# Kernel optimization log

Measured on AMD Instinct MI355X. Metric: run time of the kernel, lower is better.

Reference implementation:

```python
import jax, jax.numpy as jnp
import numpy as np

ATTEN_SIZE = 16
HIDDEN = 512


def setup_inputs() -> dict:
    key = jax.random.key(0)
    ks = jax.random.split(key, 6)
    B, S, D_in, H, D_out = 64, 100, 256, HIDDEN, 256
    # xavier-normal-ish scale for weights
    def xav(k, shape):
        fan_in, fan_out = shape
        std = np.sqrt(2.0 / (fan_in + fan_out))
        return jax.random.normal(k, shape, dtype=jnp.float32) * std
    return {
        "x": jax.random.normal(ks[0], (B, S, D_in), dtype=jnp.float32),
        "W0": xav(ks[1], (D_in, H)),
        "b0": jnp.zeros((1, 1, H), dtype=jnp.float32),
        "Wq": xav(ks[2], (H, H)),
        "Wk": xav(ks[3], (H, H)),
        "Wv": xav(ks[4], (H, H)),
        "W1": xav(ks[5], (H, D_out)),
        "b1": jnp.zeros((1, 1, D_out), dtype=jnp.float32),
    }


def reference(x, W0, b0, Wq, Wk, Wv, W1, b1):
    w = ATTEN_SIZE
    win = 2 * w + 1
    B, S = x.shape[0], x.shape[1]
    # pre-attention MLP layer (atten_layer_index = 1)
    h = jax.nn.relu(x @ W0 + b0)  # [B, S, H]
    # sliding-window neighbor gather, matching pad + roll(k) + stack + slice:
    # x_nei[:, i, k_idx] = padded[:, i + 2w - k_idx]  (reversed window order)
    padded = jnp.pad(h, ((0, 0), (w, w), (0, 0)))  # [B, S+2w, H]
    idx = jnp.arange(S)[:, None] + (2 * w - jnp.arange(win))[None, :]
    x_nei = padded[:, idx]
    q = x_nei @ Wq
    k = x_nei @ Wk
    v = x_nei @ Wv
    d = jnp.einsum('bswh,buh_->bswu'.replace('h_', 'sh'[1] + 'h'), q, k) if False else jnp.einsum('bswh,bsuh->bswu', q, k)
    d = d / jnp.sqrt(jnp.float32(HIDDEN))
    alpha = jax.nn.softmax(d, axis=-1)
    wv = jnp.einsum('bswu,bsuh->bswh', alpha, v)
    out = wv.sum(axis=2)  # sum over window rows -> [B, S, H]
    y = jax.nn.relu(out @ W1 + b1)  # [B, S, D_out]
    return y, alpha.reshape(B * S, win, win)
```

## Files before the change

kernel.cpp:

```cpp
#include <hip/hip_runtime.h>

typedef __bf16 bf16x8 __attribute__((ext_vector_type(8)));
typedef float f32x4 __attribute__((ext_vector_type(4)));
typedef unsigned int u32;

__device__ __forceinline__ unsigned short f2bf(float f) {
  unsigned int u = __float_as_uint(f);
  u += 0x7FFFu + ((u >> 16) & 1u);
  return (unsigned short)(u >> 16);
}
__device__ __forceinline__ float bf2f(unsigned short s) {
  return __uint_as_float(((unsigned int)s) << 16);
}

__device__ __forceinline__ void gload16(const void* g, void* l) {
  __builtin_amdgcn_global_load_lds(
      (const __attribute__((address_space(1))) u32*)g,
      (__attribute__((address_space(3))) u32*)l, 16, 0, 0);
}

__global__ __launch_bounds__(256) void prep_kernel(
    const float* __restrict__ x, const float* __restrict__ W0,
    const float* __restrict__ Wq, const float* __restrict__ Wk,
    const float* __restrict__ Wv, const float* __restrict__ W1,
    unsigned short* __restrict__ xb, unsigned short* __restrict__ w0t,
    unsigned short* __restrict__ wqkvt, unsigned short* __restrict__ w1t)
{
  __shared__ float tile[32][33];
  const int bid = blockIdx.x, tid = threadIdx.x;
  if (bid < 1600) {
    long i = (long)bid * 1024 + tid * 4;
    float4 v = *(const float4*)(x + i);
    ushort4 o = {f2bf(v.x), f2bf(v.y), f2bf(v.z), f2bf(v.w)};
    *(ushort4*)(xb + i) = o;
    return;
  }
  int id = bid - 1600;
  const float* src; unsigned short* dst;
  int N, DLD, k0, n0, drow0;
  if (id < 128) {
    src = W0; N = 512; dst = w0t; DLD = 256;
    k0 = (id >> 4) * 32; n0 = (id & 15) * 32; drow0 = n0;
  } else if (id < 896) {
    int id1 = id - 128, which = id1 >> 8, rem = id1 & 255;
    src = (which == 0) ? Wq : (which == 1) ? Wk : Wv;
    N = 512; dst = wqkvt; DLD = 512;
    k0 = (rem >> 4) * 32; n0 = (rem & 15) * 32; drow0 = which * 512 + n0;
  } else {
    int id2 = id - 896;
    src = W1; N = 256; dst = w1t; DLD = 512;
    k0 = (id2 >> 3) * 32; n0 = (id2 & 7) * 32; drow0 = n0;
  }
  const int tr = tid >> 5, tc = tid & 31;
#pragma unroll
  for (int rr = 0; rr < 4; ++rr) {
    int kl = tr + rr * 8;
    tile[kl][tc] = src[(long)(k0 + kl) * N + n0 + tc];
  }
  __syncthreads();
#pragma unroll
  for (int rr = 0; rr < 4; ++rr) {
    int nl = tr + rr * 8;
    dst[(long)(drow0 + nl) * DLD + k0 + tc] = f2bf(tile[tc][nl]);
  }
}

template<bool RELU, bool OUT_BF16>
__global__ __launch_bounds__(256) void gemm_tile(
    const unsigned short* __restrict__ A, int lda,
    const unsigned short* __restrict__ Bt, int ldb,
    const float* __restrict__ bias,
    void* __restrict__ Cout, int ldc, int KT)
{
  __shared__ unsigned short As[2][64 * 32];
  __shared__ unsigned short Bs[2][128 * 32];
  const int tid = threadIdx.x;
  const int m0 = blockIdx.x * 64;
  const int n0 = blockIdx.y * 128;
  const int w = tid >> 6, lane = tid & 63;
  const int lr = lane & 15, kq = lane >> 4;
  const int cg  = (tid & 3) ^ ((tid >> 3) & 3);
  const int kqs = kq ^ ((lr >> 1) & 3);

  const unsigned short* Ag  = A  + (long)(m0 + (tid >> 2)) * lda + cg * 8;
  const unsigned short* Bg0 = Bt + (long)(n0 + (tid >> 2)) * ldb + cg * 8;
  const unsigned short* Bg1 = Bg0 + (long)64 * ldb;

  f32x4 acc[4][2];
#pragma unroll
  for (int i = 0; i < 4; i++)
#pragma unroll
    for (int j = 0; j < 2; j++) acc[i][j] = (f32x4){0.f, 0.f, 0.f, 0.f};

#define STAGE(buf, kt) do { int ko = (kt) * 32;                      \
    gload16(Ag + ko,  &As[buf][tid * 8]);                            \
    gload16(Bg0 + ko, &Bs[buf][tid * 8]);                            \
    gload16(Bg1 + ko, &Bs[buf][(tid + 256) * 8]); } while (0)

  STAGE(0, 0);
  __syncthreads();
  int cur = 0;
  for (int kt = 0; kt < KT; ++kt) {
    if (kt + 1 < KT) STAGE(cur ^ 1, kt + 1);
    bf16x8 af[4], bfr[2];
#pragma unroll
    for (int ii = 0; ii < 4; ii++)
      af[ii] = *(const bf16x8*)&As[cur][(16 * ii + lr) * 32 + 8 * kqs];
#pragma unroll
    for (int jj = 0; jj < 2; jj++)
      bfr[jj] = *(const bf16x8*)&Bs[cur][(w * 32 + 16 * jj + lr) * 32 + 8 * kqs];
#pragma unroll
    for (int ii = 0; ii < 4; ii++)
#pragma unroll
      for (int jj = 0; jj < 2; jj++)
        acc[ii][jj] = __builtin_amdgcn_mfma_f32_16x16x32_bf16(af[ii], bfr[jj], acc[ii][jj], 0, 0, 0);
    __syncthreads();
    cur ^= 1;
  }
#undef STAGE

#pragma unroll
  for (int ii = 0; ii < 4; ii++) {
#pragma unroll
    for (int jj = 0; jj < 2; jj++) {
      int col = n0 + w * 32 + 16 * jj + lr;
      float bv = bias ? bias[col] : 0.0f;
#pragma unroll
      for (int r = 0; r < 4; r++) {
        int row = m0 + 16 * ii + 4 * kq + r;
        float v = acc[ii][jj][r] + bv;
        if (RELU) v = fmaxf(v, 0.0f);
        if (OUT_BF16) ((unsigned short*)Cout)[(long)row * ldc + col] = f2bf(v);
        else          ((float*)Cout)[(long)row * ldc + col] = v;
      }
    }
  }
}

__global__ __launch_bounds__(256) void gram_tile(
    const unsigned short* __restrict__ qkv, float* __restrict__ G)
{
  const float scale = 0.044194173824159216f;
  __shared__ unsigned short As[2][64 * 32];
  __shared__ unsigned short Bs[2][128 * 32];
  const int tid = threadIdx.x;
  const int m0 = blockIdx.x * 64;
  const int b  = blockIdx.y;
  const int w = tid >> 6, lane = tid & 63;
  const int lr = lane & 15, kq = lane >> 4;
  const int cg  = (tid & 3) ^ ((tid >> 3) & 3);
  const int kqs = kq ^ ((lr >> 1) & 3);

  const unsigned short* A  = qkv + (long)b * 100 * 1536;
  const unsigned short* Bt = A + 512;
  const unsigned short* Ag  = A  + (long)(m0 + (tid >> 2)) * 1536 + cg * 8;
  const unsigned short* Bg0 = Bt + (long)(tid >> 2) * 1536 + cg * 8;
  const unsigned short* Bg1 = Bg0 + (long)64 * 1536;

  f32x4 acc[4][2];
#pragma unroll
  for (int i = 0; i < 4; i++)
#pragma unroll
    for (int j = 0; j < 2; j++) acc[i][j] = (f32x4){0.f, 0.f, 0.f, 0.f};

#define STAGE(buf, kt) do { int ko = (kt) * 32;                      \
    gload16(Ag + ko,  &As[buf][tid * 8]);                            \
    gload16(Bg0 + ko, &Bs[buf][tid * 8]);                            \
    gload16(Bg1 + ko, &Bs[buf][(tid + 256) * 8]); } while (0)

  STAGE(0, 0);
  __syncthreads();
  int cur = 0;
  for (int kt = 0; kt < 16; ++kt) {
    if (kt + 1 < 16) STAGE(cur ^ 1, kt + 1);
    bf16x8 af[4], bfr[2];
#pragma unroll
    for (int ii = 0; ii < 4; ii++)
      af[ii] = *(const bf16x8*)&As[cur][(16 * ii + lr) * 32 + 8 * kqs];
#pragma unroll
    for (int jj = 0; jj < 2; jj++)
      bfr[jj] = *(const bf16x8*)&Bs[cur][(w * 32 + 16 * jj + lr) * 32 + 8 * kqs];
#pragma unroll
    for (int ii = 0; ii < 4; ii++)
#pragma unroll
      for (int jj = 0; jj < 2; jj++)
        acc[ii][jj] = __builtin_amdgcn_mfma_f32_16x16x32_bf16(af[ii], bfr[jj], acc[ii][jj], 0, 0, 0);
    __syncthreads();
    cur ^= 1;
  }
#undef STAGE

  float* Gb = G + (long)b * 10000;
#pragma unroll
  for (int ii = 0; ii < 4; ii++) {
#pragma unroll
    for (int jj = 0; jj < 2; jj++) {
      int j = w * 32 + 16 * jj + lr;
#pragma unroll
      for (int r = 0; r < 4; r++) {
        int i = m0 + 16 * ii + 4 * kq + r;
        if (i < 100 && j < 100) Gb[i * 100 + j] = acc[ii][jj][r] * scale;
      }
    }
  }
}

__global__ __launch_bounds__(256) void attn_kernel(
    const float* __restrict__ G,
    const unsigned short* __restrict__ qkv,
    float* __restrict__ alpha_out,
    unsigned short* __restrict__ outb)
{
  const int blk = blockIdx.x;
  const int b = blk / 100, s = blk % 100;
  __shared__ float dmat[33][36];
  __shared__ float rowinv[33];
  __shared__ float beta[36];
  const int tid = threadIdx.x;
  const float* Gb = G + (long)b * 10000;

  for (int t = tid; t < 1089; t += 256) {
    int dw = t / 33, du = t % 33;
    int i = s + 16 - dw, j = s + 16 - du;
    float v = 0.f;
    if ((unsigned)i < 100u && (unsigned)j < 100u) v = Gb[i * 100 + j];
    dmat[dw][du] = __expf(v);
  }
  __syncthreads();

  if (tid < 132) {
    int row = tid >> 2, g = tid & 3;
    float ssum = 0.f;
    for (int u = g; u < 33; u += 4) ssum += dmat[row][u];
    ssum += __shfl_xor(ssum, 1);
    ssum += __shfl_xor(ssum, 2);
    if (g == 0) rowinv[row] = 1.0f / ssum;
  }
  __syncthreads();

  float* aout = alpha_out + (long)blk * 1089;
  for (int t = tid; t < 1089; t += 256) {
    int dw = t / 33, du = t % 33;
    float a = dmat[dw][du] * rowinv[dw];
    aout[t] = a;
    dmat[dw][du] = a;
  }
  __syncthreads();

  if (tid < 132) {
    int col = tid >> 2, g = tid & 3;
    float sum = 0.f;
    for (int w = g; w < 33; w += 4) sum += dmat[w][col];
    sum += __shfl_xor(sum, 1);
    sum += __shfl_xor(sum, 2);
    if (g == 0) beta[col] = sum;
  }
  __syncthreads();

  const unsigned short* vbase = qkv + (long)(b * 100) * 1536 + 1024;
  {
    float acc0 = 0.f, acc1 = 0.f;
    for (int u = 0; u < 33; ++u) {
      int p = s + 16 - u;
      if ((unsigned)p < 100u) {
        float bw = beta[u];
        u32 pv = *(const u32*)(vbase + (long)p * 1536 + 2 * tid);
        acc0 += bw * bf2f((unsigned short)(pv & 0xFFFFu));
        acc1 += bw * bf2f((unsigned short)(pv >> 16));
      }
    }
    u32 packed = (u32)f2bf(acc0) | ((u32)f2bf(acc1) << 16);
    *(u32*)(outb + (long)blk * 512 + 2 * tid) = packed;
  }
}

extern "C" void kernel_launch(void* const* d_in, const int* in_sizes, int n_in,
                              void* d_out, int out_size, void* d_ws, size_t ws_size,
                              hipStream_t stream) {
  const float* x  = (const float*)d_in[0];
  const float* W0 = (const float*)d_in[1];
  const float* b0 = (const float*)d_in[2];
  const float* Wq = (const float*)d_in[3];
  const float* Wk = (const float*)d_in[4];
  const float* Wv = (const float*)d_in[5];
  const float* W1 = (const float*)d_in[6];
  const float* b1 = (const float*)d_in[7];

  char* ws = (char*)d_ws;
  unsigned short* xb    = (unsigned short*)(ws + 0);
  unsigned short* w0t   = (unsigned short*)(ws + 3276800);
  unsigned short* wqkvt = (unsigned short*)(ws + 3538944);
  unsigned short* w1t   = (unsigned short*)(ws + 5111808);
  unsigned short* h     = (unsigned short*)(ws + 5373952);
  unsigned short* qkv   = (unsigned short*)(ws + 11927552);
  float*          G     = (float*)(ws + 31686656);
  unsigned short* outb  = (unsigned short*)(ws + 34246656);

  float* y_out     = (float*)d_out;
  float* alpha_out = y_out + 6400 * 256;

  prep_kernel<<<2624, 256, 0, stream>>>(x, W0, Wq, Wk, Wv, W1, xb, w0t, wqkvt, w1t);
  gemm_tile<true,  true ><<<dim3(100, 4),  256, 0, stream>>>(xb, 256, w0t, 256, b0, h, 512, 8);
  gemm_tile<false, true ><<<dim3(100, 12), 256, 0, stream>>>(h, 512, wqkvt, 512, nullptr, qkv, 1536, 16);
  gram_tile<<<dim3(2, 64), 256, 0, stream>>>(qkv, G);
  attn_kernel<<<6400, 256, 0, stream>>>(G, qkv, alpha_out, outb);
  gemm_tile<true,  false><<<dim3(100, 2),  256, 0, stream>>>(outb, 512, w1t, 512, b1, y_out, 256, 16);
}
```

Before: 176.5 us.

## Fuse Gram-matrix and windowed softmax attention into one kernel per position block

Replaces the separate gram_tile and attn_kernel launches with a single fused_attn kernel. Each of 256 blocks computes a 64x64 local QK^T tile for 25 query positions plus their window halo, exponentiates it in shared memory, then derives row normalisers, alpha and column sums (beta) for the whole block. Out-of-range halo rows get exp(0)=1, which matches zero padding. This removes the global G round trip and the 6400-block launch. In exchange, parallelism drops to 256 blocks, and each thread runs a serial 25-position loop for the V-weighted sum. The halo loads also read qkv rows outside the batch, which are masked afterwards.

```diff
diff --git a/kernel.cpp b/kernel.cpp
--- a/kernel.cpp
+++ b/kernel.cpp
@@ -8,9 +8,6 @@
   unsigned int u = __float_as_uint(f);
   u += 0x7FFFu + ((u >> 16) & 1u);
   return (unsigned short)(u >> 16);
-}
-__device__ __forceinline__ float bf2f(unsigned short s) {
-  return __uint_as_float(((unsigned int)s) << 16);
 }
 
 __device__ __forceinline__ void gload16(const void* g, void* l) {
@@ -137,140 +134,115 @@
   }
 }
 
-__global__ __launch_bounds__(256) void gram_tile(
-    const unsigned short* __restrict__ qkv, float* __restrict__ G)
+__global__ __launch_bounds__(256) void fused_attn(
+    const unsigned short* __restrict__ qkv,
+    float* __restrict__ alpha_out,
+    unsigned short* __restrict__ outb)
 {
   const float scale = 0.044194173824159216f;
   __shared__ unsigned short As[2][64 * 32];
-  __shared__ unsigned short Bs[2][128 * 32];
+  __shared__ unsigned short Bs[2][64 * 32];
+  __shared__ float E[64][68];
+  __shared__ float rinvs[25][36];
+  __shared__ float betas[25][36];
+
   const int tid = threadIdx.x;
-  const int m0 = blockIdx.x * 64;
+  const int s0 = blockIdx.x * 25;
   const int b  = blockIdx.y;
+  const int i0 = s0 - 16;
   const int w = tid >> 6, lane = tid & 63;
   const int lr = lane & 15, kq = lane >> 4;
   const int cg  = (tid & 3) ^ ((tid >> 3) & 3);
   const int kqs = kq ^ ((lr >> 1) & 3);
 
-  const unsigned short* A  = qkv + (long)b * 100 * 1536;
-  const unsigned short* Bt = A + 512;
-  const unsigned short* Ag  = A  + (long)(m0 + (tid >> 2)) * 1536 + cg * 8;
-  const unsigned short* Bg0 = Bt + (long)(tid >> 2) * 1536 + cg * 8;
-  const unsigned short* Bg1 = Bg0 + (long)64 * 1536;
-
-  f32x4 acc[4][2];
-#pragma unroll
-  for (int i = 0; i < 4; i++)
-#pragma unroll
-    for (int j = 0; j < 2; j++) acc[i][j] = (f32x4){0.f, 0.f, 0.f, 0.f};
-
-#define STAGE(buf, kt) do { int ko = (kt) * 32;                      \
-    gload16(Ag + ko,  &As[buf][tid * 8]);                            \
-    gload16(Bg0 + ko, &Bs[buf][tid * 8]);                            \
-    gload16(Bg1 + ko, &Bs[buf][(tid + 256) * 8]); } while (0)
-
-  STAGE(0, 0);
+  const unsigned short* rowbase =
+      qkv + ((long)(b * 100 + i0 + (tid >> 2))) * 1536 + cg * 8;
+
+  f32x4 acc[4];
+#pragma unroll
+  for (int j = 0; j < 4; j++) acc[j] = (f32x4){0.f, 0.f, 0.f, 0.f};
+
+#define STAGEA(buf, kt) do { int ko = (kt) * 32;                     \
+    gload16(rowbase + ko,       &As[buf][tid * 8]);                  \
+    gload16(rowbase + 512 + ko, &Bs[buf][tid * 8]); } while (0)
+
+  STAGEA(0, 0);
   __syncthreads();
   int cur = 0;
   for (int kt = 0; kt < 16; ++kt) {
-    if (kt + 1 < 16) STAGE(cur ^ 1, kt + 1);
-    bf16x8 af[4], bfr[2];
-#pragma unroll
-    for (int ii = 0; ii < 4; ii++)
-      af[ii] = *(const bf16x8*)&As[cur][(16 * ii + lr) * 32 + 8 * kqs];
-#pragma unroll
-    for (int jj = 0; jj < 2; jj++)
-      bfr[jj] = *(const bf16x8*)&Bs[cur][(w * 32 + 16 * jj + lr) * 32 + 8 * kqs];
-#pragma unroll
-    for (int ii = 0; ii < 4; ii++)
-#pragma unroll
-      for (int jj = 0; jj < 2; jj++)
-        acc[ii][jj] = __builtin_amdgcn_mfma_f32_16x16x32_bf16(af[ii], bfr[jj], acc[ii][jj], 0, 0, 0);
+    if (kt + 1 < 16) STAGEA(cur ^ 1, kt + 1);
+    bf16x8 aq = *(const bf16x8*)&As[cur][(16 * w + lr) * 32 + 8 * kqs];
+    bf16x8 bk[4];
+#pragma unroll
+    for (int jj = 0; jj < 4; jj++)
+      bk[jj] = *(const bf16x8*)&Bs[cur][(16 * jj + lr) * 32 + 8 * kqs];
+#pragma unroll
+    for (int jj = 0; jj < 4; jj++)
+      acc[jj] = __builtin_amdgcn_mfma_f32_16x16x32_bf16(aq, bk[jj], acc[jj], 0, 0, 0);
     __syncthreads();
     cur ^= 1;
   }
-#undef STAGE
-
-  float* Gb = G + (long)b * 10000;
-#pragma unroll
-  for (int ii = 0; ii < 4; ii++) {
-#pragma unroll
-    for (int jj = 0; jj < 2; jj++) {
-      int j = w * 32 + 16 * jj + lr;
-#pragma unroll
-      for (int r = 0; r < 4; r++) {
-        int i = m0 + 16 * ii + 4 * kq + r;
-        if (i < 100 && j < 100) Gb[i * 100 + j] = acc[ii][jj][r] * scale;
+#undef STAGEA
+
+#pragma unroll
+  for (int jj = 0; jj < 4; jj++) {
+    int jl = 16 * jj + lr;
+    bool jok = (unsigned)(i0 + jl) < 100u;
+#pragma unroll
+    for (int r = 0; r < 4; r++) {
+      int il = 16 * w + 4 * kq + r;
+      bool iok = (unsigned)(i0 + il) < 100u;
+      E[il][jl] = (iok && jok) ? __expf(scale * acc[jj][r]) : 1.0f;
+    }
+  }
+  __syncthreads();
+
+  for (int task = tid; task < 825; task += 256) {
+    int si = task / 33, dw = task % 33;
+    int il = si + 32 - dw;
+    float sum = 0.f;
+    const float* er = &E[il][si];
+#pragma unroll
+    for (int t = 0; t < 33; ++t) sum += er[t];
+    rinvs[si][dw] = 1.0f / sum;
+  }
+  __syncthreads();
+
+  if (tid < 231) {
+    int sg = tid / 33, du = tid % 33;
+#pragma unroll
+    for (int k = 0; k < 4; ++k) {
+      int si = sg + 7 * k;
+      if (si < 25) {
+        float bsum = 0.f;
+        float* aout = alpha_out + (long)(b * 100 + s0 + si) * 1089 + du;
+        int jl = si + 32 - du;
+        for (int dw = 0; dw < 33; ++dw) {
+          float a = E[si + 32 - dw][jl] * rinvs[si][dw];
+          aout[dw * 33] = a;
+          bsum += a;
+        }
+        betas[si][du] = bsum;
       }
     }
   }
-}
-
-__global__ __launch_bounds__(256) void attn_kernel(
-    const float* __restrict__ G,
-    const unsigned short* __restrict__ qkv,
-    float* __restrict__ alpha_out,
-    unsigned short* __restrict__ outb)
-{
-  const int blk = blockIdx.x;
-  const int b = blk / 100, s = blk % 100;
-  __shared__ float dmat[33][36];
-  __shared__ float rowinv[33];
-  __shared__ float beta[36];
-  const int tid = threadIdx.x;
-  const float* Gb = G + (long)b * 10000;
-
-  for (int t = tid; t < 1089; t += 256) {
-    int dw = t / 33, du = t % 33;
-    int i = s + 16 - dw, j = s + 16 - du;
-    float v = 0.f;
-    if ((unsigned)i < 100u && (unsigned)j < 100u) v = Gb[i * 100 + j];
-    dmat[dw][du] = __expf(v);
-  }
-  __syncthreads();
-
-  if (tid < 132) {
-    int row = tid >> 2, g = tid & 3;
-    float ssum = 0.f;
-    for (int u = g; u < 33; u += 4) ssum += dmat[row][u];
-    ssum += __shfl_xor(ssum, 1);
-    ssum += __shfl_xor(ssum, 2);
-    if (g == 0) rowinv[row] = 1.0f / ssum;
-  }
-  __syncthreads();
-
-  float* aout = alpha_out + (long)blk * 1089;
-  for (int t = tid; t < 1089; t += 256) {
-    int dw = t / 33, du = t % 33;
-    float a = dmat[dw][du] * rowinv[dw];
-    aout[t] = a;
-    dmat[dw][du] = a;
-  }
-  __syncthreads();
-
-  if (tid < 132) {
-    int col = tid >> 2, g = tid & 3;
-    float sum = 0.f;
-    for (int w = g; w < 33; w += 4) sum += dmat[w][col];
-    sum += __shfl_xor(sum, 1);
-    sum += __shfl_xor(sum, 2);
-    if (g == 0) beta[col] = sum;
-  }
   __syncthreads();
 
   const unsigned short* vbase = qkv + (long)(b * 100) * 1536 + 1024;
-  {
+  for (int si = 0; si < 25; ++si) {
     float acc0 = 0.f, acc1 = 0.f;
+    int s = s0 + si;
     for (int u = 0; u < 33; ++u) {
       int p = s + 16 - u;
       if ((unsigned)p < 100u) {
-        float bw = beta[u];
+        float bw = betas[si][u];
         u32 pv = *(const u32*)(vbase + (long)p * 1536 + 2 * tid);
-        acc0 += bw * bf2f((unsigned short)(pv & 0xFFFFu));
-        acc1 += bw * bf2f((unsigned short)(pv >> 16));
+        acc0 = fmaf(bw, __uint_as_float(pv << 16), acc0);
+        acc1 = fmaf(bw, __uint_as_float(pv & 0xFFFF0000u), acc1);
       }
     }
     u32 packed = (u32)f2bf(acc0) | ((u32)f2bf(acc1) << 16);
-    *(u32*)(outb + (long)blk * 512 + 2 * tid) = packed;
+    *(u32*)(outb + (long)(b * 100 + s) * 512 + 2 * tid) = packed;
   }
 }
 
@@ -293,8 +265,7 @@
   unsigned short* w1t   = (unsigned short*)(ws + 5111808);
   unsigned short* h     = (unsigned short*)(ws + 5373952);
   unsigned short* qkv   = (unsigned short*)(ws + 11927552);
-  float*          G     = (float*)(ws + 31686656);
-  unsigned short* outb  = (unsigned short*)(ws + 34246656);
+  unsigned short* outb  = (unsigned short*)(ws + 31686656);
 
   float* y_out     = (float*)d_out;
   float* alpha_out = y_out + 6400 * 256;
@@ -302,7 +273,6 @@
   prep_kernel<<<2624, 256, 0, stream>>>(x, W0, Wq, Wk, Wv, W1, xb, w0t, wqkvt, w1t);
   gemm_tile<true,  true ><<<dim3(100, 4),  256, 0, stream>>>(xb, 256, w0t, 256, b0, h, 512, 8);
   gemm_tile<false, true ><<<dim3(100, 12), 256, 0, stream>>>(h, 512, wqkvt, 512, nullptr, qkv, 1536, 16);
-  gram_tile<<<dim3(2, 64), 256, 0, stream>>>(qkv, G);
-  attn_kernel<<<6400, 256, 0, stream>>>(G, qkv, alpha_out, outb);
+  fused_attn<<<dim3(4, 64), 256, 0, stream>>>(qkv, alpha_out, outb);
   gemm_tile<true,  false><<<dim3(100, 2),  256, 0, stream>>>(outb, 512, w1t, 512, b1, y_out, 256, 16);
 }
```

Result: slower. 240.5 us (+36.2%).
